# Kernel optimization log

Hardware: AMD Instinct MI355X
Metric: run time of the kernel (lower is better)

The kernel has to match this reference:

```python
import jax, jax.numpy as jnp
import numpy as np

D_K = 64

def setup_inputs() -> dict:
    key = jax.random.key(0)
    kq, kk, kv = jax.random.split(key, 3)
    shape = (2, 16, 2048, D_K)  # [B, H, S, d_k]
    q = jax.random.normal(kq, shape, dtype=jnp.float32)
    k = jax.random.normal(kk, shape, dtype=jnp.float32)
    v = jax.random.normal(kv, shape, dtype=jnp.float32)
    return {"q": q, "k": k, "v": v}

def reference(q, k, v):
    # score = q @ k^T / sqrt(d_k)  -> [B, H, S, S]
    scale = 1.0 / np.sqrt(D_K).astype(np.float32)
    score = jnp.einsum("bhqd,bhkd->bhqk", q, k) * scale
    attn = jax.nn.softmax(score, axis=-1)
    # dropout is identity in eval mode
    out = jnp.einsum("bhqk,bhkd->bhqd", attn, v)
    return out
```

## Files before the change

### kernel.cpp

```cpp
#include <hip/hip_runtime.h>
#include <hip/hip_bf16.h>
#include <math.h>
#include <stdint.h>


#define S_LEN 2048
#define DK 64
#define QW 32
#define NW 4
#define QBLK (QW * NW)
#define KVBLK 64
#define NT (S_LEN / KVBLK)
#define LOG2E 1.44269504088896340736f
#define THR 8.0f

typedef __attribute__((ext_vector_type(16))) float f32x16;
typedef __attribute__((ext_vector_type(8)))  __bf16 bf16x8;
typedef __attribute__((ext_vector_type(4)))  __bf16 bf16x4;
typedef __attribute__((ext_vector_type(4)))  uint32_t u32x4;

union frag_cast { u32x4 u; bf16x8 h; };

__device__ __forceinline__ uint32_t cvt_pk_bf16(float lo, float hi) {
    uint32_t r;
    asm("v_cvt_pk_bf16_f32 %0, %1, %2" : "=v"(r) : "v"(lo), "v"(hi));
    return r;
}
__device__ __forceinline__ void perm32swap(uint32_t& a, uint32_t& b) {
    asm volatile("v_permlane32_swap_b32 %0, %1" : "+v"(a), "+v"(b));
}
__device__ __forceinline__ void load_lds16(const __bf16* g, __bf16* l) {
    __builtin_amdgcn_global_load_lds(
        (const __attribute__((address_space(1))) void*)g,
        (__attribute__((address_space(3))) void*)l, 16, 0, 0);
}
__device__ __forceinline__ bf16x8 pack8(float4 a, float4 b) {
    bf16x8 f;
    f[0] = (__bf16)a.x; f[1] = (__bf16)a.y; f[2] = (__bf16)a.z; f[3] = (__bf16)a.w;
    f[4] = (__bf16)b.x; f[5] = (__bf16)b.y; f[6] = (__bf16)b.z; f[7] = (__bf16)b.w;
    return f;
}

__global__ __launch_bounds__(256)
void prep_pack(const float* __restrict__ Kg, const float* __restrict__ Vg,
               __bf16* __restrict__ Kimg, __bf16* __restrict__ Vimg)
{
    __shared__ float Vs[64 * 65];
    const int tid = threadIdx.x;
    const int t = blockIdx.x, bh = blockIdx.y;
    const size_t ibase = ((size_t)bh * S_LEN + (size_t)t * 64) * DK;
    const size_t obase = ((size_t)bh * NT + t) * 4096;

    #pragma unroll
    for (int u0 = 0; u0 < 2; ++u0) {
        const int u = tid + 256 * u0;
        const int f = u >> 6, lane = u & 63;
        const int sp = f >> 1, kt2 = f & 1;
        const int row = kt2 * 32 + (lane & 31);
        const int col = 16 * sp + 8 * (lane >> 5);
        const float* src = Kg + ibase + row * 64 + col;
        float4 a = *(const float4*)(src);
        float4 b = *(const float4*)(src + 4);
        *(bf16x8*)(Kimg + obase + (size_t)u * 8) = pack8(a, b);
    }

    {
        const int r = tid >> 2, c0 = (tid & 3) * 16;
        const float* src = Vg + ibase + r * 64 + c0;
        #pragma unroll
        for (int m = 0; m < 4; ++m) {
            float4 x = *(const float4*)(src + 4 * m);
            float* dst = &Vs[r * 65 + c0 + 4 * m];
            dst[0] = x.x; dst[1] = x.y; dst[2] = x.z; dst[3] = x.w;
        }
    }
    __syncthreads();
    #pragma unroll
    for (int u0 = 0; u0 < 2; ++u0) {
        const int u = tid + 256 * u0;
        const int g = u >> 6, lane = u & 63;
        const int ks = g >> 1, dt = g & 1;
        const int k0 = 16 * ks + 8 * (lane >> 5);
        const int d  = dt * 32 + (lane & 31);
        bf16x8 wv;
        #pragma unroll
        for (int i = 0; i < 8; ++i) wv[i] = (__bf16)Vs[(k0 + i) * 65 + d];
        *(bf16x8*)(Vimg + obase + (size_t)u * 8) = wv;
    }
}

__global__ __launch_bounds__(256, 2)
void attn_fwd_lds(const float* __restrict__ Qg, const __bf16* __restrict__ Kimg,
                  const __bf16* __restrict__ Vimg, float* __restrict__ Og)
{
    __shared__ __align__(16) __bf16 Kl[3][4096];
    __shared__ __align__(16) __bf16 Vt[3][4096];

    const int tid = threadIdx.x;
    const int lane = tid & 63;
    const int w   = tid >> 6;
    const int l31 = lane & 31;
    const int hi  = lane >> 5;

    int qt, bh;
    {
        const int lin = blockIdx.y * gridDim.x + blockIdx.x;
        if (gridDim.x * gridDim.y == 512) {
            const int xcd = lin & 7, slot = lin >> 3;
            bh = xcd * 4 + (slot >> 4);
            qt = slot & 15;
        } else { qt = blockIdx.x; bh = blockIdx.y; }
    }

    const size_t base = (size_t)bh * (S_LEN * DK);
    const int q0g = qt * QBLK + w * QW;

    bf16x8 qf[4];
    {
        const float sc = 0.125f * LOG2E;
        const float* qrow = Qg + base + (size_t)(q0g + l31) * DK;
        #pragma unroll
        for (int sp = 0; sp < 4; ++sp) {
            const int d0 = 16 * sp + 8 * hi;
            float4 a = *(const float4*)(qrow + d0);
            float4 b = *(const float4*)(qrow + d0 + 4);
            bf16x8 f;
            f[0] = (__bf16)(a.x * sc); f[1] = (__bf16)(a.y * sc);
            f[2] = (__bf16)(a.z * sc); f[3] = (__bf16)(a.w * sc);
            f[4] = (__bf16)(b.x * sc); f[5] = (__bf16)(b.y * sc);
            f[6] = (__bf16)(b.z * sc); f[7] = (__bf16)(b.w * sc);
            qf[sp] = f;
        }
    }

    bf16x8 ones;
    #pragma unroll
    for (int i = 0; i < 8; ++i) ones[i] = (__bf16)1.0f;

    f32x16 acc0 = {}, acc1 = {}, acc2 = {};
    float m_run = -INFINITY;

    const __bf16* kbase = Kimg + (size_t)bh * NT * 4096;
    const __bf16* vbase = Vimg + (size_t)bh * NT * 4096;
    const int loff = lane * 8;

    auto stage = [&](int t, int b) {
        const __bf16* kt = kbase + (size_t)t * 4096 + tid * 8;
        const __bf16* vt = vbase + (size_t)t * 4096 + tid * 8;
        load_lds16(kt,        &Kl[b][w * 512]);
        load_lds16(kt + 2048, &Kl[b][2048 + w * 512]);
        load_lds16(vt,        &Vt[b][w * 512]);
        load_lds16(vt + 2048, &Vt[b][2048 + w * 512]);
    };

    stage(0, 0);
    stage(1, 1);
    asm volatile("s_waitcnt vmcnt(4)" ::: "memory");
    __builtin_amdgcn_s_barrier();
    __builtin_amdgcn_sched_barrier(0);

    int cur = 0, nxt = 1, nn = 2;
    #pragma unroll 1
    for (int t = 0; t < NT; ++t) {
        if (t + 2 < NT) stage(t + 2, nn);

        f32x16 s0 = {}, s1 = {};
        __builtin_amdgcn_s_setprio(1);
        #pragma unroll
        for (int sp = 0; sp < 4; ++sp) {
            bf16x8 kb0 = *(const bf16x8*)(&Kl[cur][(sp * 2 + 0) * 512 + loff]);
            bf16x8 kb1 = *(const bf16x8*)(&Kl[cur][(sp * 2 + 1) * 512 + loff]);
            s0 = __builtin_amdgcn_mfma_f32_32x32x16_bf16(kb0, qf[sp], s0, 0, 0, 0);
            s1 = __builtin_amdgcn_mfma_f32_32x32x16_bf16(kb1, qf[sp], s1, 0, 0, 0);
        }
        __builtin_amdgcn_s_setprio(0);

        float a16[16];
        #pragma unroll
        for (int j = 0; j < 16; ++j) a16[j] = fmaxf(s0[j], s1[j]);
        float vmax = fmaxf(fmaxf(a16[0], a16[1]), a16[2]);
        #pragma unroll
        for (int j = 0; j < 6; ++j)
            vmax = fmaxf(fmaxf(vmax, a16[3 + 2 * j]), a16[4 + 2 * j]);
        vmax = fmaxf(vmax, a16[15]);
        vmax = fmaxf(vmax, __shfl_xor(vmax, 32));

        if (!__all(vmax - m_run <= THR)) {
            const float mnew = fmaxf(m_run, vmax);
            const float alpha = __builtin_amdgcn_exp2f(m_run - mnew);
            m_run = mnew;
            #pragma unroll
            for (int r = 0; r < 16; ++r) {
                const int ql = (r & 3) + 8 * (r >> 2) + 4 * hi;
                const float ar = __shfl(alpha, ql + (hi << 5));
                acc0[r] *= ar;
                acc1[r] *= ar;
                acc2[r] *= ar;
            }
        }

        #pragma unroll
        for (int j = 0; j < 16; ++j) s0[j] = __builtin_amdgcn_exp2f(s0[j] - m_run);
        #pragma unroll
        for (int j = 0; j < 16; ++j) s1[j] = __builtin_amdgcn_exp2f(s1[j] - m_run);

        frag_cast pa[4];
        #pragma unroll
        for (int b2 = 0; b2 < 2; ++b2) {
            #pragma unroll
            for (int st = 0; st < 2; ++st) {
                uint32_t wa, wb, wc, wd;
                if (b2 == 0) {
                    wa = cvt_pk_bf16(s0[8 * st + 0], s0[8 * st + 1]);
                    wb = cvt_pk_bf16(s0[8 * st + 2], s0[8 * st + 3]);
                    wc = cvt_pk_bf16(s0[8 * st + 4], s0[8 * st + 5]);
                    wd = cvt_pk_bf16(s0[8 * st + 6], s0[8 * st + 7]);
                } else {
                    wa = cvt_pk_bf16(s1[8 * st + 0], s1[8 * st + 1]);
                    wb = cvt_pk_bf16(s1[8 * st + 2], s1[8 * st + 3]);
                    wc = cvt_pk_bf16(s1[8 * st + 4], s1[8 * st + 5]);
                    wd = cvt_pk_bf16(s1[8 * st + 6], s1[8 * st + 7]);
                }
                perm32swap(wa, wc);
                perm32swap(wb, wd);
                pa[2 * b2 + st].u = (u32x4){wa, wb, wc, wd};
            }
        }

        __builtin_amdgcn_s_setprio(1);
        #pragma unroll
        for (int ks = 0; ks < 4; ++ks) {
            bf16x8 vb0 = *(const bf16x8*)(&Vt[cur][(ks * 2 + 0) * 512 + loff]);
            bf16x8 vb1 = *(const bf16x8*)(&Vt[cur][(ks * 2 + 1) * 512 + loff]);
            acc0 = __builtin_amdgcn_mfma_f32_32x32x16_bf16(pa[ks].h, vb0, acc0, 0, 0, 0);
            acc1 = __builtin_amdgcn_mfma_f32_32x32x16_bf16(pa[ks].h, vb1, acc1, 0, 0, 0);
            acc2 = __builtin_amdgcn_mfma_f32_32x32x16_bf16(pa[ks].h, ones, acc2, 0, 0, 0);
        }
        __builtin_amdgcn_s_setprio(0);

        if (t + 2 < NT) {
            asm volatile("s_waitcnt vmcnt(4)" ::: "memory");
        } else if (t + 1 < NT) {
            asm volatile("s_waitcnt vmcnt(0)" ::: "memory");
        }
        if (t + 1 < NT) {
            __builtin_amdgcn_s_barrier();
            __builtin_amdgcn_sched_barrier(0);
        }
        const int tmp = cur; cur = nxt; nxt = nn; nn = tmp;
    }

    float* op = Og + base;
    #pragma unroll
    for (int r = 0; r < 16; ++r) {
        const int ql = (r & 3) + 8 * (r >> 2) + 4 * hi;
        const float invl = 1.0f / acc2[r];
        const size_t row = (size_t)(q0g + ql) * DK;
        op[row + l31]      = acc0[r] * invl;
        op[row + 32 + l31] = acc1[r] * invl;
    }
}

__global__ __launch_bounds__(256, 2)
void attn_fwd_fb(const float* __restrict__ Qg, const float* __restrict__ Kg,
                 const float* __restrict__ Vg, float* __restrict__ Og)
{
    __shared__ __align__(16) __bf16 Kl[2][64 * 64];
    __shared__ __align__(16) __bf16 Vt[2][64 * 64];

    const int tid = threadIdx.x;
    const int lane = tid & 63;
    const int w   = tid >> 6;
    const int l31 = lane & 31;
    const int hi  = lane >> 5;

    const int qt = blockIdx.x;
    const int bh = blockIdx.y;
    const size_t base = (size_t)bh * (S_LEN * DK);
    const int q0g = qt * QBLK + w * QW;

    bf16x8 qf[4];
    {
        const float sc = 0.125f * LOG2E;
        const float* qrow = Qg + base + (size_t)(q0g + l31) * DK;
        #pragma unroll
        for (int sp = 0; sp < 4; ++sp) {
            const int d0 = 16 * sp + 8 * hi;
            float4 a = *(const float4*)(qrow + d0);
            float4 b = *(const float4*)(qrow + d0 + 4);
            bf16x8 f;
            f[0] = (__bf16)(a.x * sc); f[1] = (__bf16)(a.y * sc);
            f[2] = (__bf16)(a.z * sc); f[3] = (__bf16)(a.w * sc);
            f[4] = (__bf16)(b.x * sc); f[5] = (__bf16)(b.y * sc);
            f[6] = (__bf16)(b.z * sc); f[7] = (__bf16)(b.w * sc);
            qf[sp] = f;
        }
    }

    f32x16 acc0 = {}, acc1 = {};
    float m_run = -INFINITY, l_run = 0.f;

    float4 kpre[4];
    float  vpre[4][4];
    const int vd  = tid & 63;
    const int vkq = tid >> 6;

    auto issueLoads = [&](int t) {
        const int kv0 = t * KVBLK;
        #pragma unroll
        for (int i = 0; i < 4; ++i) {
            const int idx = tid + 256 * i;
            const int r = idx >> 4, c = idx & 15;
            kpre[i] = *(const float4*)(Kg + base + (size_t)(kv0 + r) * DK + c * 4);
        }
        #pragma unroll
        for (int i = 0; i < 4; ++i) {
            const int k0 = vkq * 4 + 16 * i;
            const float* vp = Vg + base + (size_t)(kv0 + k0) * DK + vd;
            vpre[i][0] = vp[0];      vpre[i][1] = vp[DK];
            vpre[i][2] = vp[2 * DK]; vpre[i][3] = vp[3 * DK];
        }
    };
    auto writeTile = [&](int b) {
        #pragma unroll
        for (int i = 0; i < 4; ++i) {
            const int idx = tid + 256 * i;
            const int r = idx >> 4, c = idx & 15;
            bf16x4 pk;
            pk[0] = (__bf16)kpre[i].x; pk[1] = (__bf16)kpre[i].y;
            pk[2] = (__bf16)kpre[i].z; pk[3] = (__bf16)kpre[i].w;
            *(bf16x4*)(&Kl[b][r * 64 + ((c * 4) ^ ((r & 7) << 3))]) = pk;
        }
        #pragma unroll
        for (int i = 0; i < 4; ++i) {
            const int k0 = vkq * 4 + 16 * i;
            bf16x4 pv;
            pv[0] = (__bf16)vpre[i][0]; pv[1] = (__bf16)vpre[i][1];
            pv[2] = (__bf16)vpre[i][2]; pv[3] = (__bf16)vpre[i][3];
            *(bf16x4*)(&Vt[b][vd * 64 + (k0 ^ ((vd & 7) << 3))]) = pv;
        }
    };

    issueLoads(0);
    writeTile(0);
    __syncthreads();

    int cur = 0;
    #pragma unroll 1
    for (int t = 0; t < NT; ++t) {
        if (t + 1 < NT) issueLoads(t + 1);

        f32x16 s0 = {}, s1 = {};
        #pragma unroll
        for (int sp = 0; sp < 4; ++sp) {
            #pragma unroll
            for (int kt2 = 0; kt2 < 2; ++kt2) {
                const int krow = kt2 * 32 + l31;
                const int eo = krow * 64 + ((16 * sp + 8 * hi) ^ ((krow & 7) << 3));
                bf16x8 kb = *(const bf16x8*)(&Kl[cur][eo]);
                if (kt2 == 0) s0 = __builtin_amdgcn_mfma_f32_32x32x16_bf16(kb, qf[sp], s0, 0, 0, 0);
                else          s1 = __builtin_amdgcn_mfma_f32_32x32x16_bf16(kb, qf[sp], s1, 0, 0, 0);
            }
        }

        float vmax = -INFINITY;
        #pragma unroll
        for (int j = 0; j < 16; ++j) vmax = fmaxf(vmax, s0[j]);
        #pragma unroll
        for (int j = 0; j < 16; ++j) vmax = fmaxf(vmax, s1[j]);
        vmax = fmaxf(vmax, __shfl_xor(vmax, 32));

        if (!__all(vmax - m_run <= THR)) {
            const float mnew = fmaxf(m_run, vmax);
            const float alpha = __builtin_amdgcn_exp2f(m_run - mnew);
            m_run = mnew;
            l_run *= alpha;
            #pragma unroll
            for (int r = 0; r < 16; ++r) {
                const int ql = (r & 3) + 8 * (r >> 2) + 4 * hi;
                const float ar = __shfl(alpha, ql + (hi << 5));
                acc0[r] *= ar;
                acc1[r] *= ar;
            }
        }

        float rs = 0.f;
        #pragma unroll
        for (int j = 0; j < 16; ++j) { const float p = __builtin_amdgcn_exp2f(s0[j] - m_run); s0[j] = p; rs += p; }
        #pragma unroll
        for (int j = 0; j < 16; ++j) { const float p = __builtin_amdgcn_exp2f(s1[j] - m_run); s1[j] = p; rs += p; }
        rs += __shfl_xor(rs, 32);
        l_run += rs;

        frag_cast pa[4];
        #pragma unroll
        for (int b2 = 0; b2 < 2; ++b2) {
            #pragma unroll
            for (int st = 0; st < 2; ++st) {
                uint32_t wa, wb, wc, wd;
                if (b2 == 0) {
                    wa = cvt_pk_bf16(s0[8 * st + 0], s0[8 * st + 1]);
                    wb = cvt_pk_bf16(s0[8 * st + 2], s0[8 * st + 3]);
                    wc = cvt_pk_bf16(s0[8 * st + 4], s0[8 * st + 5]);
                    wd = cvt_pk_bf16(s0[8 * st + 6], s0[8 * st + 7]);
                } else {
                    wa = cvt_pk_bf16(s1[8 * st + 0], s1[8 * st + 1]);
                    wb = cvt_pk_bf16(s1[8 * st + 2], s1[8 * st + 3]);
                    wc = cvt_pk_bf16(s1[8 * st + 4], s1[8 * st + 5]);
                    wd = cvt_pk_bf16(s1[8 * st + 6], s1[8 * st + 7]);
                }
                perm32swap(wa, wc);
                perm32swap(wb, wd);
                pa[2 * b2 + st].u = (u32x4){wa, wb, wc, wd};
            }
        }

        #pragma unroll
        for (int ks = 0; ks < 4; ++ks) {
            #pragma unroll
            for (int dt = 0; dt < 2; ++dt) {
                const int d = dt * 32 + l31;
                const int eo = d * 64 + ((16 * ks + 8 * hi) ^ ((d & 7) << 3));
                bf16x8 vb = *(const bf16x8*)(&Vt[cur][eo]);
                if (dt == 0) acc0 = __builtin_amdgcn_mfma_f32_32x32x16_bf16(pa[ks].h, vb, acc0, 0, 0, 0);
                else         acc1 = __builtin_amdgcn_mfma_f32_32x32x16_bf16(pa[ks].h, vb, acc1, 0, 0, 0);
            }
        }

        if (t + 1 < NT) writeTile(cur ^ 1);
        __syncthreads();
        cur ^= 1;
    }

    float* op = Og + base;
    #pragma unroll
    for (int r = 0; r < 16; ++r) {
        const int ql = (r & 3) + 8 * (r >> 2) + 4 * hi;
        const float lr = __shfl(l_run, ql + (hi << 5));
        const float invl = 1.0f / lr;
        const size_t row = (size_t)(q0g + ql) * DK;
        op[row + l31]      = acc0[r] * invl;
        op[row + 32 + l31] = acc1[r] * invl;
    }
}

extern "C" void kernel_launch(void* const* d_in, const int* in_sizes, int n_in,
                              void* d_out, int out_size, void* d_ws, size_t ws_size,
                              hipStream_t stream) {
    const float* q = (const float*)d_in[0];
    const float* k = (const float*)d_in[1];
    const float* v = (const float*)d_in[2];
    float* o = (float*)d_out;
    const int bh = in_sizes[0] / (S_LEN * DK);

    const size_t img_bytes = (size_t)bh * NT * 4096 * sizeof(__bf16);
    if (ws_size >= 2 * img_bytes) {
        __bf16* Kimg = (__bf16*)d_ws;
        __bf16* Vimg = (__bf16*)((char*)d_ws + img_bytes);
        prep_pack<<<dim3(NT, bh), dim3(256), 0, stream>>>(k, v, Kimg, Vimg);
        attn_fwd_lds<<<dim3(S_LEN / QBLK, bh), dim3(256), 0, stream>>>(q, Kimg, Vimg, o);
    } else {
        attn_fwd_fb<<<dim3(S_LEN / QBLK, bh), dim3(256), 0, stream>>>(q, k, v, o);
    }
}
```

Before: 68.78 us.

## Split KV range across two wave groups per block and merge partial softmax

Doubles the block to 512 threads, with two groups of four waves each processing half of the key/value tiles for the same 128 queries. Each group keeps its own online-softmax state. At the end, group 1 writes its partial output, max and denominator to LDS and group 0 rescales and merges them before writing. This raises the number of waves per CU to hide latency on a grid of only 512 blocks. In exchange it drops from triple to double buffering with a full block barrier per tile, and adds an LDS merge step.

```diff
diff --git a/kernel.cpp b/kernel.cpp
--- a/kernel.cpp
+++ b/kernel.cpp
@@ -7,10 +7,11 @@
 #define S_LEN 2048
 #define DK 64
 #define QW 32
-#define NW 4
-#define QBLK (QW * NW)
+#define QBLK 128
 #define KVBLK 64
 #define NT (S_LEN / KVBLK)
+#define KVSPLIT 2
+#define NTG (NT / KVSPLIT)
 #define LOG2E 1.44269504088896340736f
 #define THR 8.0f
 
@@ -89,18 +90,26 @@
     }
 }
 
-__global__ __launch_bounds__(256, 2)
+__global__ __launch_bounds__(512, 4)
 void attn_fwd_lds(const float* __restrict__ Qg, const __bf16* __restrict__ Kimg,
                   const __bf16* __restrict__ Vimg, float* __restrict__ Og)
 {
-    __shared__ __align__(16) __bf16 Kl[3][4096];
-    __shared__ __align__(16) __bf16 Vt[3][4096];
-
-    const int tid = threadIdx.x;
+    __shared__ __align__(16) unsigned char smem[65536];
+    __bf16* KlBase = (__bf16*)smem;
+    __bf16* VtBase = (__bf16*)(smem + 32768);
+    float* O1p = (float*)smem;
+    float* m0a = (float*)(smem + 32768);
+    float* m1a = (float*)(smem + 32768 + 512);
+    float* l1a = (float*)(smem + 32768 + 1024);
+
+    const int tid  = threadIdx.x;
     const int lane = tid & 63;
-    const int w   = tid >> 6;
-    const int l31 = lane & 31;
-    const int hi  = lane >> 5;
+    const int wv   = tid >> 6;
+    const int qg   = wv & 3;
+    const int g    = wv >> 2;
+    const int gtid = tid & 255;
+    const int l31  = lane & 31;
+    const int hi   = lane >> 5;
 
     int qt, bh;
     {
@@ -113,7 +122,7 @@
     }
 
     const size_t base = (size_t)bh * (S_LEN * DK);
-    const int q0g = qt * QBLK + w * QW;
+    const int q0g = qt * QBLK + qg * QW;
 
     bf16x8 qf[4];
     {
@@ -143,33 +152,36 @@
     const __bf16* kbase = Kimg + (size_t)bh * NT * 4096;
     const __bf16* vbase = Vimg + (size_t)bh * NT * 4096;
     const int loff = lane * 8;
-
-    auto stage = [&](int t, int b) {
-        const __bf16* kt = kbase + (size_t)t * 4096 + tid * 8;
-        const __bf16* vt = vbase + (size_t)t * 4096 + tid * 8;
-        load_lds16(kt,        &Kl[b][w * 512]);
-        load_lds16(kt + 2048, &Kl[b][2048 + w * 512]);
-        load_lds16(vt,        &Vt[b][w * 512]);
-        load_lds16(vt + 2048, &Vt[b][2048 + w * 512]);
+    const int t0 = g * NTG;
+
+    auto stage = [&](int tl, int b) {
+        const __bf16* kt = kbase + (size_t)(t0 + tl) * 4096 + gtid * 8;
+        const __bf16* vt = vbase + (size_t)(t0 + tl) * 4096 + gtid * 8;
+        __bf16* kd = KlBase + (size_t)(g * 2 + b) * 4096;
+        __bf16* vd = VtBase + (size_t)(g * 2 + b) * 4096;
+        load_lds16(kt,        kd + qg * 512);
+        load_lds16(kt + 2048, kd + 2048 + qg * 512);
+        load_lds16(vt,        vd + qg * 512);
+        load_lds16(vt + 2048, vd + 2048 + qg * 512);
     };
 
     stage(0, 0);
-    stage(1, 1);
-    asm volatile("s_waitcnt vmcnt(4)" ::: "memory");
-    __builtin_amdgcn_s_barrier();
-    __builtin_amdgcn_sched_barrier(0);
-
-    int cur = 0, nxt = 1, nn = 2;
+    __syncthreads();
+
+    int cur = 0;
     #pragma unroll 1
-    for (int t = 0; t < NT; ++t) {
-        if (t + 2 < NT) stage(t + 2, nn);
+    for (int tl = 0; tl < NTG; ++tl) {
+        if (tl + 1 < NTG) stage(tl + 1, cur ^ 1);
+
+        const __bf16* Kc = KlBase + (size_t)(g * 2 + cur) * 4096;
+        const __bf16* Vc = VtBase + (size_t)(g * 2 + cur) * 4096;
 
         f32x16 s0 = {}, s1 = {};
         __builtin_amdgcn_s_setprio(1);
         #pragma unroll
         for (int sp = 0; sp < 4; ++sp) {
-            bf16x8 kb0 = *(const bf16x8*)(&Kl[cur][(sp * 2 + 0) * 512 + loff]);
-            bf16x8 kb1 = *(const bf16x8*)(&Kl[cur][(sp * 2 + 1) * 512 + loff]);
+            bf16x8 kb0 = *(const bf16x8*)(&Kc[(sp * 2 + 0) * 512 + loff]);
+            bf16x8 kb1 = *(const bf16x8*)(&Kc[(sp * 2 + 1) * 512 + loff]);
             s0 = __builtin_amdgcn_mfma_f32_32x32x16_bf16(kb0, qf[sp], s0, 0, 0, 0);
             s1 = __builtin_amdgcn_mfma_f32_32x32x16_bf16(kb1, qf[sp], s1, 0, 0, 0);
         }
@@ -230,34 +242,57 @@
         __builtin_amdgcn_s_setprio(1);
         #pragma unroll
         for (int ks = 0; ks < 4; ++ks) {
-            bf16x8 vb0 = *(const bf16x8*)(&Vt[cur][(ks * 2 + 0) * 512 + loff]);
-            bf16x8 vb1 = *(const bf16x8*)(&Vt[cur][(ks * 2 + 1) * 512 + loff]);
+            bf16x8 vb0 = *(const bf16x8*)(&Vc[(ks * 2 + 0) * 512 + loff]);
+            bf16x8 vb1 = *(const bf16x8*)(&Vc[(ks * 2 + 1) * 512 + loff]);
             acc0 = __builtin_amdgcn_mfma_f32_32x32x16_bf16(pa[ks].h, vb0, acc0, 0, 0, 0);
             acc1 = __builtin_amdgcn_mfma_f32_32x32x16_bf16(pa[ks].h, vb1, acc1, 0, 0, 0);
             acc2 = __builtin_amdgcn_mfma_f32_32x32x16_bf16(pa[ks].h, ones, acc2, 0, 0, 0);
         }
         __builtin_amdgcn_s_setprio(0);
 
-        if (t + 2 < NT) {
-            asm volatile("s_waitcnt vmcnt(4)" ::: "memory");
-        } else if (t + 1 < NT) {
-            asm volatile("s_waitcnt vmcnt(0)" ::: "memory");
-        }
-        if (t + 1 < NT) {
-            __builtin_amdgcn_s_barrier();
-            __builtin_amdgcn_sched_barrier(0);
-        }
-        const int tmp = cur; cur = nxt; nxt = nn; nn = tmp;
-    }
-
-    float* op = Og + base;
-    #pragma unroll
-    for (int r = 0; r < 16; ++r) {
-        const int ql = (r & 3) + 8 * (r >> 2) + 4 * hi;
-        const float invl = 1.0f / acc2[r];
-        const size_t row = (size_t)(q0g + ql) * DK;
-        op[row + l31]      = acc0[r] * invl;
-        op[row + 32 + l31] = acc1[r] * invl;
+        __syncthreads();
+        cur ^= 1;
+    }
+
+    if (g == 1) {
+        #pragma unroll
+        for (int r = 0; r < 16; ++r) {
+            const int ql = (r & 3) + 8 * (r >> 2) + 4 * hi;
+            const int row = qg * 32 + ql;
+            O1p[row * 64 + l31]      = acc0[r];
+            O1p[row * 64 + 32 + l31] = acc1[r];
+        }
+        if (hi == 0) m1a[qg * 32 + l31] = m_run;
+        if (l31 == 0) {
+            #pragma unroll
+            for (int r = 0; r < 16; ++r) {
+                const int ql = (r & 3) + 8 * (r >> 2) + 4 * hi;
+                l1a[qg * 32 + ql] = acc2[r];
+            }
+        }
+    } else {
+        if (hi == 0) m0a[qg * 32 + l31] = m_run;
+    }
+    __syncthreads();
+
+    if (g == 0) {
+        float* op = Og + base;
+        #pragma unroll
+        for (int r = 0; r < 16; ++r) {
+            const int ql = (r & 3) + 8 * (r >> 2) + 4 * hi;
+            const int row = qg * 32 + ql;
+            const float m0r = m0a[row], m1r = m1a[row];
+            const float mr = fmaxf(m0r, m1r);
+            const float a0 = __builtin_amdgcn_exp2f(m0r - mr);
+            const float a1 = __builtin_amdgcn_exp2f(m1r - mr);
+            const float lr = acc2[r] * a0 + l1a[row] * a1;
+            const float invl = 1.0f / lr;
+            const float o0 = acc0[r] * a0 + O1p[row * 64 + l31] * a1;
+            const float o1 = acc1[r] * a0 + O1p[row * 64 + 32 + l31] * a1;
+            const size_t orow = (size_t)(q0g + ql) * DK;
+            op[orow + l31]      = o0 * invl;
+            op[orow + 32 + l31] = o1 * invl;
+        }
     }
 }
 
@@ -458,7 +493,7 @@
         __bf16* Kimg = (__bf16*)d_ws;
         __bf16* Vimg = (__bf16*)((char*)d_ws + img_bytes);
         prep_pack<<<dim3(NT, bh), dim3(256), 0, stream>>>(k, v, Kimg, Vimg);
-        attn_fwd_lds<<<dim3(S_LEN / QBLK, bh), dim3(256), 0, stream>>>(q, Kimg, Vimg, o);
+        attn_fwd_lds<<<dim3(S_LEN / QBLK, bh), dim3(512), 0, stream>>>(q, Kimg, Vimg, o);
     } else {
         attn_fwd_fb<<<dim3(S_LEN / QBLK, bh), dim3(256), 0, stream>>>(q, k, v, o);
     }
```

After: 65.73 us. 4.4% less time.
